# Kernel optimization log

Hardware: AMD Instinct MI355X
Metric: run time of the kernel (lower is better)

## Reference

```python
import jax, jax.numpy as jnp
import numpy as np

N = 8192
D_IN = 512
D_OUT = 128
DENSITY = 0.004  # avg degree ~32
NEG_INF = -1.0e10
LEAKY_ALPHA = 0.2  # tf.nn.leaky_relu default


def setup_inputs() -> dict:
    key = jax.random.key(0)
    k_x, k_adj, k_w, k_as, k_an = jax.random.split(key, 5)
    x = jax.random.normal(k_x, (N, D_IN), dtype=jnp.float32)
    # sparse binary adjacency, materialized dense (as the module does via tf.sparse.to_dense)
    adj = (jax.random.uniform(k_adj, (N, N)) < DENSITY).astype(jnp.float32)
    adj = jnp.maximum(adj, jnp.eye(N, dtype=jnp.float32))  # self-loops so softmax rows are valid
    W = jax.random.normal(k_w, (D_IN, D_OUT), dtype=jnp.float32) * (1.0 / np.sqrt(D_IN))
    attn_self = jax.random.normal(k_as, (D_OUT, 1), dtype=jnp.float32) * 0.1
    attn_neigh = jax.random.normal(k_an, (D_OUT, 1), dtype=jnp.float32) * 0.1
    return {"x": x, "adj": adj, "W": W, "attn_self": attn_self, "attn_neigh": attn_neigh}


def reference(x, adj, W, attn_self, attn_neigh):
    # dropouts are 0.0 -> identity
    h = x @ W                                   # [N, D_OUT]
    a_s = h @ attn_self                          # [N, 1]
    a_n = h @ attn_neigh                         # [N, 1]
    e = a_s + a_n.T                              # [N, N] additive attention logits
    e = jnp.where(e >= 0, e, LEAKY_ALPHA * e)    # leaky_relu
    e = e + NEG_INF * (1.0 - adj)                # mask non-edges
    attn = jax.nn.softmax(e, axis=-1)            # row-wise softmax [N, N]
    out = attn @ h                               # [N, D_OUT]
    return jax.nn.relu(out)
```

## Files before the change

### kernel.cpp

```cpp
#include <hip/hip_runtime.h>
#include <hip/hip_bf16.h>
#include <cstdint>

#define NN 8192
#define DIN 512
#define DOUT 128
#define NEG_SLOPE 0.2f
#define MAXE 256

typedef float fvec4 __attribute__((ext_vector_type(4)));

__device__ inline fvec4 ntload4(const float* p) {
#if __has_builtin(__builtin_nontemporal_load)
    return __builtin_nontemporal_load((const fvec4*)p);
#else
    return *(const fvec4*)p;
#endif
}

__global__ __launch_bounds__(256) void k_gemm_h(
    const float* __restrict__ x, const float* __restrict__ W,
    const float* __restrict__ attn_self, const float* __restrict__ attn_neigh,
    float* __restrict__ h, float* __restrict__ a_s, float* __restrict__ a_n) {
    __shared__ float4 xs[8 * 128];
    const int tid = threadIdx.x;
    const int m0 = blockIdx.x * 8;
    const float4* x4 = (const float4*)(x + (size_t)m0 * DIN);
#pragma unroll
    for (int r = 0; r < 4; ++r) xs[tid + 256 * r] = x4[tid + 256 * r];
    __syncthreads();

    const int c4 = tid & 31;
    const int rg = tid >> 5;
    const float4* W4 = (const float4*)W;
    const float4* xr = xs + rg * 128;
    float4 acc = {0.f, 0.f, 0.f, 0.f};
#pragma unroll 4
    for (int k4 = 0; k4 < 128; ++k4) {
        float4 xv = xr[k4];
        float4 w0 = W4[(4 * k4 + 0) * 32 + c4];
        float4 w1 = W4[(4 * k4 + 1) * 32 + c4];
        float4 w2 = W4[(4 * k4 + 2) * 32 + c4];
        float4 w3 = W4[(4 * k4 + 3) * 32 + c4];
        acc.x += xv.x * w0.x + xv.y * w1.x + xv.z * w2.x + xv.w * w3.x;
        acc.y += xv.x * w0.y + xv.y * w1.y + xv.z * w2.y + xv.w * w3.y;
        acc.z += xv.x * w0.z + xv.y * w1.z + xv.z * w2.z + xv.w * w3.z;
        acc.w += xv.x * w0.w + xv.y * w1.w + xv.z * w2.w + xv.w * w3.w;
    }
    const int row = m0 + rg;
    ((float4*)h)[(size_t)row * 32 + c4] = acc;

    float4 as4 = ((const float4*)attn_self)[c4];
    float4 an4 = ((const float4*)attn_neigh)[c4];
    float ps = acc.x * as4.x + acc.y * as4.y + acc.z * as4.z + acc.w * as4.w;
    float pn = acc.x * an4.x + acc.y * an4.y + acc.z * an4.z + acc.w * an4.w;
#pragma unroll
    for (int off = 16; off > 0; off >>= 1) {
        ps += __shfl_xor(ps, off);
        pn += __shfl_xor(pn, off);
    }
    if (c4 == 0) { a_s[row] = ps; a_n[row] = pn; }
}

__global__ __launch_bounds__(256) void k_attn(
    const float* __restrict__ adj, const float* __restrict__ h,
    const float* __restrict__ a_s, const float* __restrict__ a_n,
    float* __restrict__ out) {
    const int i = blockIdx.x;
    const int tid = threadIdx.x;
    __shared__ int s_cnt;
    __shared__ int s_idx[MAXE];
    __shared__ float s_w[MAXE];
    __shared__ float s_red[4];
    __shared__ float s_red2[4];
    __shared__ float s_acc[256];
    if (tid == 0) s_cnt = 0;
    const float asi = a_s[i];
    __syncthreads();

    const float* arow = adj + ((size_t)i << 13);
    fvec4 v[8];
#pragma unroll
    for (int r = 0; r < 8; ++r) v[r] = ntload4(arow + 4 * (tid + 256 * r));
#pragma unroll
    for (int r = 0; r < 8; ++r) {
        int base = (tid + 256 * r) * 4;
#pragma unroll
        for (int q = 0; q < 4; ++q) {
            if (v[r][q] != 0.f) {
                int j = base + q;
                float e = asi + a_n[j];
                e = (e >= 0.f) ? e : NEG_SLOPE * e;
                int p = atomicAdd(&s_cnt, 1);
                if (p < MAXE) { s_idx[p] = j; s_w[p] = e; }
            }
        }
    }
    __syncthreads();
    const int cnt = min(s_cnt, MAXE);

    float m = -1e30f;
    for (int t = tid; t < cnt; t += 256) m = fmaxf(m, s_w[t]);
#pragma unroll
    for (int off = 32; off > 0; off >>= 1) m = fmaxf(m, __shfl_xor(m, off));
    if ((tid & 63) == 0) s_red[tid >> 6] = m;
    __syncthreads();
    m = fmaxf(fmaxf(s_red[0], s_red[1]), fmaxf(s_red[2], s_red[3]));

    float lsum = 0.f;
    for (int t = tid; t < cnt; t += 256) {
        float w = __expf(s_w[t] - m);
        s_w[t] = w;
        lsum += w;
    }
#pragma unroll
    for (int off = 32; off > 0; off >>= 1) lsum += __shfl_xor(lsum, off);
    if ((tid & 63) == 0) s_red2[tid >> 6] = lsum;
    __syncthreads();
    const float inv_d = 1.0f / (s_red2[0] + s_red2[1] + s_red2[2] + s_red2[3]);

    const int c = tid & 127;
    const int half = tid >> 7;
    float acc = 0.f;
    int t = half;
    for (; t + 6 < cnt; t += 8) {
        float w0 = s_w[t];     int j0 = s_idx[t];
        float w1 = s_w[t + 2]; int j1 = s_idx[t + 2];
        float w2 = s_w[t + 4]; int j2 = s_idx[t + 4];
        float w3 = s_w[t + 6]; int j3 = s_idx[t + 6];
        float h0 = h[(size_t)j0 * DOUT + c];
        float h1 = h[(size_t)j1 * DOUT + c];
        float h2 = h[(size_t)j2 * DOUT + c];
        float h3 = h[(size_t)j3 * DOUT + c];
        acc += w0 * h0 + w1 * h1 + w2 * h2 + w3 * h3;
    }
    for (; t < cnt; t += 2) acc += s_w[t] * h[(size_t)s_idx[t] * DOUT + c];

    s_acc[tid] = acc;
    __syncthreads();
    if (tid < 128) {
        float tot = (s_acc[tid] + s_acc[tid + 128]) * inv_d;
        out[(size_t)i * DOUT + tid] = fmaxf(tot, 0.f);
    }
}

extern "C" void kernel_launch(void* const* d_in, const int* in_sizes, int n_in,
                              void* d_out, int out_size, void* d_ws, size_t ws_size,
                              hipStream_t stream) {
    const float* x          = (const float*)d_in[0];
    const float* adj        = (const float*)d_in[1];
    const float* W          = (const float*)d_in[2];
    const float* attn_self  = (const float*)d_in[3];
    const float* attn_neigh = (const float*)d_in[4];
    float* out = (float*)d_out;

    float* h   = (float*)d_ws;
    float* a_s = h + (size_t)NN * DOUT;
    float* a_n = a_s + NN;

    hipLaunchKernelGGL(k_gemm_h, dim3(NN / 8), dim3(256), 0, stream,
                       x, W, attn_self, attn_neigh, h, a_s, a_n);
    hipLaunchKernelGGL(k_attn, dim3(NN), dim3(256), 0, stream, adj, h, a_s, a_n, out);
}
```

Baseline: 423.4 us.

## Overlap adjacency compaction with the projection GEMM in a single launch

Moves the dense adjacency scan and neighbour-index compaction out of the attention kernel into the first launch, so it runs in extra blocks alongside the x@W GEMM blocks. Compacted indices and counts go to workspace, and a second kernel computes the logits, softmax and aggregation from that edge list. The intent is to hide the 256MB adjacency read behind the GEMM instead of running it after. It adds an index write and read through global memory and needs more workspace.

```diff
diff --git a/kernel.cpp b/kernel.cpp
--- a/kernel.cpp
+++ b/kernel.cpp
@@ -7,6 +7,7 @@
 #define DOUT 128
 #define NEG_SLOPE 0.2f
 #define MAXE 256
+#define GEMM_BLOCKS 1024
 
 typedef float fvec4 __attribute__((ext_vector_type(4)));
 
@@ -18,89 +19,107 @@
 #endif
 }
 
-__global__ __launch_bounds__(256) void k_gemm_h(
+__global__ __launch_bounds__(256) void k_fused(
     const float* __restrict__ x, const float* __restrict__ W,
     const float* __restrict__ attn_self, const float* __restrict__ attn_neigh,
-    float* __restrict__ h, float* __restrict__ a_s, float* __restrict__ a_n) {
-    __shared__ float4 xs[8 * 128];
+    const float* __restrict__ adj,
+    float* __restrict__ h, float* __restrict__ a_s, float* __restrict__ a_n,
+    int* __restrict__ e_cnt, int* __restrict__ e_idx) {
+    __shared__ char smem_raw[16384];
+    __shared__ int s_cnt;
     const int tid = threadIdx.x;
-    const int m0 = blockIdx.x * 8;
-    const float4* x4 = (const float4*)(x + (size_t)m0 * DIN);
+    const int bid = blockIdx.x;
+
+    if (bid < GEMM_BLOCKS) {
+        float4* xs = (float4*)smem_raw;
+        const int m0 = bid * 8;
+        const float4* x4 = (const float4*)(x + (size_t)m0 * DIN);
 #pragma unroll
-    for (int r = 0; r < 4; ++r) xs[tid + 256 * r] = x4[tid + 256 * r];
-    __syncthreads();
+        for (int r = 0; r < 4; ++r) xs[tid + 256 * r] = x4[tid + 256 * r];
+        __syncthreads();
 
-    const int c4 = tid & 31;
-    const int rg = tid >> 5;
-    const float4* W4 = (const float4*)W;
-    const float4* xr = xs + rg * 128;
-    float4 acc = {0.f, 0.f, 0.f, 0.f};
+        const int c4 = tid & 31;
+        const int rg = tid >> 5;
+        const float4* W4 = (const float4*)W;
+        const float4* xr = xs + rg * 128;
+        float4 acc = {0.f, 0.f, 0.f, 0.f};
 #pragma unroll 4
-    for (int k4 = 0; k4 < 128; ++k4) {
-        float4 xv = xr[k4];
-        float4 w0 = W4[(4 * k4 + 0) * 32 + c4];
-        float4 w1 = W4[(4 * k4 + 1) * 32 + c4];
-        float4 w2 = W4[(4 * k4 + 2) * 32 + c4];
-        float4 w3 = W4[(4 * k4 + 3) * 32 + c4];
-        acc.x += xv.x * w0.x + xv.y * w1.x + xv.z * w2.x + xv.w * w3.x;
-        acc.y += xv.x * w0.y + xv.y * w1.y + xv.z * w2.y + xv.w * w3.y;
-        acc.z += xv.x * w0.z + xv.y * w1.z + xv.z * w2.z + xv.w * w3.z;
-        acc.w += xv.x * w0.w + xv.y * w1.w + xv.z * w2.w + xv.w * w3.w;
+        for (int k4 = 0; k4 < 128; ++k4) {
+            float4 xv = xr[k4];
+            float4 w0 = W4[(4 * k4 + 0) * 32 + c4];
+            float4 w1 = W4[(4 * k4 + 1) * 32 + c4];
+            float4 w2 = W4[(4 * k4 + 2) * 32 + c4];
+            float4 w3 = W4[(4 * k4 + 3) * 32 + c4];
+            acc.x += xv.x * w0.x + xv.y * w1.x + xv.z * w2.x + xv.w * w3.x;
+            acc.y += xv.x * w0.y + xv.y * w1.y + xv.z * w2.y + xv.w * w3.y;
+            acc.z += xv.x * w0.z + xv.y * w1.z + xv.z * w2.z + xv.w * w3.z;
+            acc.w += xv.x * w0.w + xv.y * w1.w + xv.z * w2.w + xv.w * w3.w;
+        }
+        const int row = m0 + rg;
+        ((float4*)h)[(size_t)row * 32 + c4] = acc;
+
+        float4 as4 = ((const float4*)attn_self)[c4];
+        float4 an4 = ((const float4*)attn_neigh)[c4];
+        float ps = acc.x * as4.x + acc.y * as4.y + acc.z * as4.z + acc.w * as4.w;
+        float pn = acc.x * an4.x + acc.y * an4.y + acc.z * an4.z + acc.w * an4.w;
+#pragma unroll
+        for (int off = 16; off > 0; off >>= 1) {
+            ps += __shfl_xor(ps, off);
+            pn += __shfl_xor(pn, off);
+        }
+        if (c4 == 0) { a_s[row] = ps; a_n[row] = pn; }
+    } else {
+        const int i = bid - GEMM_BLOCKS;
+        int* s_idx = (int*)smem_raw;
+        if (tid == 0) s_cnt = 0;
+        __syncthreads();
+
+        const float* arow = adj + ((size_t)i << 13);
+        fvec4 v[8];
+#pragma unroll
+        for (int r = 0; r < 8; ++r) v[r] = ntload4(arow + 4 * (tid + 256 * r));
+#pragma unroll
+        for (int r = 0; r < 8; ++r) {
+            int base = (tid + 256 * r) * 4;
+#pragma unroll
+            for (int q = 0; q < 4; ++q) {
+                if (v[r][q] != 0.f) {
+                    int p = atomicAdd(&s_cnt, 1);
+                    if (p < MAXE) s_idx[p] = base + q;
+                }
+            }
+        }
+        __syncthreads();
+        const int cnt = min(s_cnt, MAXE);
+        for (int t = tid; t < cnt; t += 256) e_idx[(size_t)i * MAXE + t] = s_idx[t];
+        if (tid == 0) e_cnt[i] = cnt;
     }
-    const int row = m0 + rg;
-    ((float4*)h)[(size_t)row * 32 + c4] = acc;
-
-    float4 as4 = ((const float4*)attn_self)[c4];
-    float4 an4 = ((const float4*)attn_neigh)[c4];
-    float ps = acc.x * as4.x + acc.y * as4.y + acc.z * as4.z + acc.w * as4.w;
-    float pn = acc.x * an4.x + acc.y * an4.y + acc.z * an4.z + acc.w * an4.w;
-#pragma unroll
-    for (int off = 16; off > 0; off >>= 1) {
-        ps += __shfl_xor(ps, off);
-        pn += __shfl_xor(pn, off);
-    }
-    if (c4 == 0) { a_s[row] = ps; a_n[row] = pn; }
 }
 
-__global__ __launch_bounds__(256) void k_attn(
-    const float* __restrict__ adj, const float* __restrict__ h,
-    const float* __restrict__ a_s, const float* __restrict__ a_n,
-    float* __restrict__ out) {
+__global__ __launch_bounds__(256) void k_soft(
+    const float* __restrict__ h, const float* __restrict__ a_s,
+    const float* __restrict__ a_n, const int* __restrict__ e_cnt,
+    const int* __restrict__ e_idx, float* __restrict__ out) {
     const int i = blockIdx.x;
     const int tid = threadIdx.x;
-    __shared__ int s_cnt;
     __shared__ int s_idx[MAXE];
     __shared__ float s_w[MAXE];
     __shared__ float s_red[4];
     __shared__ float s_red2[4];
     __shared__ float s_acc[256];
-    if (tid == 0) s_cnt = 0;
+
+    const int cnt = e_cnt[i];
     const float asi = a_s[i];
-    __syncthreads();
-
-    const float* arow = adj + ((size_t)i << 13);
-    fvec4 v[8];
-#pragma unroll
-    for (int r = 0; r < 8; ++r) v[r] = ntload4(arow + 4 * (tid + 256 * r));
-#pragma unroll
-    for (int r = 0; r < 8; ++r) {
-        int base = (tid + 256 * r) * 4;
-#pragma unroll
-        for (int q = 0; q < 4; ++q) {
-            if (v[r][q] != 0.f) {
-                int j = base + q;
-                float e = asi + a_n[j];
-                e = (e >= 0.f) ? e : NEG_SLOPE * e;
-                int p = atomicAdd(&s_cnt, 1);
-                if (p < MAXE) { s_idx[p] = j; s_w[p] = e; }
-            }
-        }
-    }
-    __syncthreads();
-    const int cnt = min(s_cnt, MAXE);
 
     float m = -1e30f;
-    for (int t = tid; t < cnt; t += 256) m = fmaxf(m, s_w[t]);
+    for (int t = tid; t < cnt; t += 256) {
+        int j = e_idx[(size_t)i * MAXE + t];
+        s_idx[t] = j;
+        float e = asi + a_n[j];
+        e = (e >= 0.f) ? e : NEG_SLOPE * e;
+        s_w[t] = e;
+        m = fmaxf(m, e);
+    }
 #pragma unroll
     for (int off = 32; off > 0; off >>= 1) m = fmaxf(m, __shfl_xor(m, off));
     if ((tid & 63) == 0) s_red[tid >> 6] = m;
@@ -157,8 +176,11 @@
     float* h   = (float*)d_ws;
     float* a_s = h + (size_t)NN * DOUT;
     float* a_n = a_s + NN;
+    int* e_cnt = (int*)(a_n + NN);
+    int* e_idx = e_cnt + NN;
 
-    hipLaunchKernelGGL(k_gemm_h, dim3(NN / 8), dim3(256), 0, stream,
-                       x, W, attn_self, attn_neigh, h, a_s, a_n);
-    hipLaunchKernelGGL(k_attn, dim3(NN), dim3(256), 0, stream, adj, h, a_s, a_n, out);
+    hipLaunchKernelGGL(k_fused, dim3(GEMM_BLOCKS + NN), dim3(256), 0, stream,
+                       x, W, attn_self, attn_neigh, adj, h, a_s, a_n, e_cnt, e_idx);
+    hipLaunchKernelGGL(k_soft, dim3(NN), dim3(256), 0, stream,
+                       h, a_s, a_n, e_cnt, e_idx, out);
 }
```

Result: no change. 415.4 us (-1.9%).
